# Kernel tuning notes

Measured on AMD Instinct MI355X. Metric: run time of the kernel, lower is better.

## Reference

```python
import jax, jax.numpy as jnp
import numpy as np
from jax import lax

KH, KW = 9, 9
FC_DIM = 1024
C_RED = FC_DIM // 8  # 128
EPS = 1e-5


def conv_bn_relu(x, w, gamma, beta):
    # 3x3 conv, stride 1, pad 1 (NCHW / OIHW), then batch-stat BN + ReLU
    y = lax.conv_general_dilated(x, w, (1, 1), ((1, 1), (1, 1)),
                                 dimension_numbers=('NCHW', 'OIHW', 'NCHW'))
    mean = y.mean(axis=(0, 2, 3))
    var = y.var(axis=(0, 2, 3))
    y = (y - mean[None, :, None, None]) * lax.rsqrt(var + EPS)[None, :, None, None]
    y = y * gamma[None, :, None, None] + beta[None, :, None, None]
    return jnp.maximum(y, 0.0)


def local_weighting(feat, atten, kH, kW):
    # feat: [B,C,H,W]; atten: [B,H,W,kH*kW]
    # out[b,c,h,w] = sum_k atten[b,h,w,k] * feat_padded[b,c,h+dh_k,w+dw_k]
    B, C, H, W = feat.shape
    ph, pw = kH // 2, kW // 2
    fp = jnp.pad(feat, ((0, 0), (0, 0), (ph, ph), (pw, pw)))
    out = jnp.zeros_like(feat)
    k = 0
    for dh in range(kH):
        for dw in range(kW):
            out = out + fp[:, :, dh:dh + H, dw:dw + W] * atten[:, None, :, :, k]
            k += 1
    return out


def setup_inputs() -> dict:
    key = jax.random.key(0)
    ks = jax.random.split(key, 12)
    B, H, W = 4, 64, 64
    sc1 = 1.0 / np.sqrt(FC_DIM * 9)
    sc5 = 1.0 / np.sqrt(C_RED * 9)
    return {
        'low_key': jax.random.normal(ks[0], (B, FC_DIM, H, W), jnp.float32),
        'low_nonkey': jax.random.normal(ks[1], (B, FC_DIM, H, W), jnp.float32),
        'local_atten': jax.random.uniform(ks[2], (B, H, W, KH * KW), jnp.float32),
        'w1': jax.random.normal(ks[3], (C_RED, FC_DIM, 3, 3), jnp.float32) * sc1,
        'g1': jnp.ones((C_RED,), jnp.float32),
        'b1': jnp.zeros((C_RED,), jnp.float32),
        'w4': jax.random.normal(ks[4], (C_RED, FC_DIM, 3, 3), jnp.float32) * sc1,
        'g4': jnp.ones((C_RED,), jnp.float32),
        'b4': jnp.zeros((C_RED,), jnp.float32),
        'w5': jax.random.normal(ks[5], (C_RED, C_RED, 3, 3), jnp.float32) * sc5,
        'g5': jnp.ones((C_RED,), jnp.float32),
        'b5': jnp.zeros((C_RED,), jnp.float32),
        'fc1_w': jax.random.normal(ks[6], (10, C_RED), jnp.float32) * (1.0 / np.sqrt(C_RED)),
        'fc1_b': jnp.zeros((10,), jnp.float32),
        'fc2_w': jax.random.normal(ks[7], (1, 10), jnp.float32) * (1.0 / np.sqrt(10.0)),
        'fc2_b': jnp.zeros((1,), jnp.float32),
    }


def reference(low_key, low_nonkey, local_atten,
              w1, g1, b1, w4, g4, b4, w5, g5, b5,
              fc1_w, fc1_b, fc2_w, fc2_b):
    lk = conv_bn_relu(low_key, w1, g1, b1)          # [B,128,H,W]
    trans = local_weighting(lk, local_atten, KH, KW)
    lnk = conv_bn_relu(low_nonkey, w4, g4, b4)
    out = trans - lnk
    out = conv_bn_relu(out, w5, g5, b5)
    out = out.mean(axis=(2, 3))                      # adaptive avg pool to 1x1 -> [B,128]
    out = out @ fc1_w.T + fc1_b
    out = out @ fc2_w.T + fc2_b                      # [B,1]
    return out
```

## Files before the change

kernel.cpp:

```cpp
#include <hip/hip_runtime.h>
#include <hip/hip_bf16.h>


#define B_ 4
#define CM_ 128

typedef __attribute__((ext_vector_type(8))) short short8;
typedef __attribute__((ext_vector_type(4))) float floatx4;
typedef __attribute__((address_space(3))) unsigned lds_as;
typedef __attribute__((address_space(1))) const unsigned glb_as;

__device__ inline short f2bf(float f) {
  union { float f; unsigned u; } v; v.f = f;
  unsigned r = v.u + 0x7fff + ((v.u >> 16) & 1);
  return (short)(r >> 16);
}
__device__ inline float bf2f(unsigned short u) {
  union { unsigned u; float f; } v; v.u = ((unsigned)u) << 16;
  return v.f;
}

template <int KB>
__global__ void xprep_kernel(const float* __restrict__ x, short* __restrict__ xt) {
  int kb = blockIdx.x >> 4, rg = blockIdx.x & 15;
  int b = blockIdx.y;
  int row = rg * 4 + (threadIdx.x >> 6);
  int col = threadIdx.x & 63;
  const float* xs = x + (((size_t)b * (KB * 32) + kb * 32) * 64 + row) * 64 + col;
  short* xd = xt + ((((size_t)b * KB + kb) * 64 + row) * 64 + col) * 32;
  int sw = (col >> 1) & 3;
#pragma unroll
  for (int u = 0; u < 4; u++) {
    short8 pk;
#pragma unroll
    for (int j = 0; j < 8; j++) pk[j] = f2bf(xs[(size_t)(u * 8 + j) * 4096]);
    *(short8*)(xd + (u ^ sw) * 8) = pk;
  }
}

__global__ void prep1_kernel(const float* __restrict__ x1,
                             const float* __restrict__ w1, const float* __restrict__ w4,
                             const float* __restrict__ w5, const float* __restrict__ atten,
                             short* __restrict__ xt, short* __restrict__ wf1,
                             short* __restrict__ wf4, short* __restrict__ wf5,
                             float* __restrict__ att_t, float* __restrict__ yz) {
  __shared__ float tile[5184];
  int bx = blockIdx.x, tid = threadIdx.x;
  if (bx < 2048) {
    int b = bx & 3, t = bx >> 2;
    int kb = t >> 4, rg = t & 15;
    int row = rg * 4 + (tid >> 6), col = tid & 63;
    const float* xs = x1 + (((size_t)b * 1024 + kb * 32) * 64 + row) * 64 + col;
    short* xd = xt + ((((size_t)b * 32 + kb) * 64 + row) * 64 + col) * 32;
    int sw = (col >> 1) & 3;
#pragma unroll
    for (int u = 0; u < 4; u++) {
      short8 pk;
#pragma unroll
      for (int j = 0; j < 8; j++) pk[j] = f2bf(xs[(size_t)(u * 8 + j) * 4096]);
      *(short8*)(xd + (u ^ sw) * 8) = pk;
    }
    return;
  }
  bx -= 2048;
  if (bx < 1024) {
    const float* w = bx < 512 ? w1 : w4;
    short* wf = bx < 512 ? wf1 : wf4;
    int idx = (bx & 511) * 256 + tid;
    int oc = idx >> 10, ic = idx & 1023;
    int kb = ic >> 5, icb = ic & 31, quad = icb >> 3, j = icb & 7;
    int m = oc >> 4, n16 = oc & 15, lane = quad * 16 + n16;
    const float* wp = w + ((size_t)oc * 1024 + ic) * 9;
    short* base = wf + (size_t)kb * 36864 + lane * 8 + j;
#pragma unroll
    for (int r = 0; r < 3; r++)
#pragma unroll
      for (int s = 0; s < 3; s++)
        base[(size_t)r * 12288 + (s * 8 + m) * 512] = f2bf(wp[r * 3 + s]);
    return;
  }
  bx -= 1024;
  if (bx < 64) {
    int idx = bx * 256 + tid;
    int oc = idx >> 7, ic = idx & 127;
    int kb = ic >> 5, icb = ic & 31, quad = icb >> 3, j = icb & 7;
    int m = oc >> 4, n16 = oc & 15, lane = quad * 16 + n16;
    const float* wp = w5 + ((size_t)oc * 128 + ic) * 9;
    short* base = wf5 + (size_t)kb * 36864 + lane * 8 + j;
#pragma unroll
    for (int r = 0; r < 3; r++)
#pragma unroll
      for (int s = 0; s < 3; s++)
        base[(size_t)r * 12288 + (s * 8 + m) * 512] = f2bf(wp[r * 3 + s]);
    return;
  }
  bx -= 64;
  if (bx < 256) {
    int b = bx >> 6;
    int p0 = (bx & 63) * 64;
    const float* src = atten + ((size_t)b * 4096 + p0) * 81;
    for (int e = tid; e < 5184; e += 256) tile[e] = src[e];
    __syncthreads();
    for (int f = tid; f < 5184; f += 256) {
      int k = f >> 6, w_ = f & 63;
      att_t[((size_t)b * 81 + k) * 4096 + p0 + w_] = tile[w_ * 81 + k];
    }
    return;
  }
  bx -= 256;
  ((float4*)yz)[(size_t)bx * 256 + tid] = make_float4(0.f, 0.f, 0.f, 0.f);
}

template <int KQ, bool ATOMIC>
__global__ __launch_bounds__(256, 2)
void convm_kernel(const short* __restrict__ xt, const short* __restrict__ wf,
                  float* __restrict__ ya, float* __restrict__ yb, int KBtot) {
  __shared__ __attribute__((aligned(16))) short smem[32768];
  int tid = threadIdx.x, lane = tid & 63, wv = tid >> 6;
  int n16 = lane & 15, quad = lane >> 4;
  int pg = blockIdx.x;
  int b = pg >> 5, h0 = (pg & 31) * 2;
  int kb0 = blockIdx.y * KQ;
  int mh = wv & 1, nh = wv >> 1;
  float* yo = ATOMIC ? ya : (blockIdx.y ? yb : ya);
  short* sx = smem + 24576;

  if (h0 == 0)
    for (int i = tid; i < 1024; i += 256) ((int*)sx)[i] = 0;
  if (h0 == 62)
    for (int i = tid; i < 1024; i += 256) ((int*)(sx + 3 * 2048))[i] = 0;

  auto dma_x = [&](int kb) {
    int row = h0 - 1 + wv;
    if (row >= 0 && row < 64) {
      const short* src = xt + ((((size_t)b * KBtot + kb) * 64 + row) * 64) * 32 + lane * 8;
      short* dst = sx + wv * 2048 + lane * 8;
#pragma unroll
      for (int t = 0; t < 4; t++)
        __builtin_amdgcn_global_load_lds((glb_as*)(src + t * 512), (lds_as*)(dst + t * 512),
                                         16, 0, 0);
    }
  };
  auto dma_w = [&](int step, int buf) {
    const short* src = wf + ((size_t)kb0 * 3 + step) * 12288 + wv * 3072 + lane * 8;
    short* dst = smem + buf * 12288 + wv * 3072 + lane * 8;
#pragma unroll
    for (int t = 0; t < 6; t++)
      __builtin_amdgcn_global_load_lds((glb_as*)(src + t * 512), (lds_as*)(dst + t * 512),
                                       16, 0, 0);
  };

  floatx4 acc[4][4];
#pragma unroll
  for (int i = 0; i < 4; i++)
#pragma unroll
    for (int n = 0; n < 4; n++) acc[i][n] = (floatx4){0.f, 0.f, 0.f, 0.f};

  dma_x(kb0);
  dma_w(0, 0);
  const int NS = KQ * 3;
  for (int s = 0; s < NS; s++) {
    int r = s % 3;
    __syncthreads();
    if (r == 0 && s > 0) {
      dma_x(kb0 + s / 3);
      if (s + 1 < NS) dma_w(s + 1, (s + 1) & 1);
      __syncthreads();
    } else {
      if (s + 1 < NS) dma_w(s + 1, (s + 1) & 1);
    }
    const short* swb = smem + (s & 1) * 12288;
    int slot = nh + r;
    const short* sxr = sx + slot * 2048;
#pragma unroll
    for (int sp = 0; sp < 3; sp++) {
      short8 a[4];
#pragma unroll
      for (int i = 0; i < 4; i++)
        a[i] = *(const short8*)(swb + ((sp * 8 + mh * 4 + i) * 64 + lane) * 8);
#pragma unroll
      for (int n = 0; n < 4; n++) {
        int c = n * 16 + n16 + sp - 1;
        int cc = c < 0 ? 0 : (c > 63 ? 63 : c);
        short8 bf = *(const short8*)(sxr + cc * 32 + (quad ^ ((cc >> 1) & 3)) * 8);
        if ((n == 0 && sp == 0) || (n == 3 && sp == 2)) {
          short8 zz = {0, 0, 0, 0, 0, 0, 0, 0};
          bf = (c != cc) ? zz : bf;
        }
#pragma unroll
        for (int i = 0; i < 4; i++)
          acc[i][n] = __builtin_amdgcn_mfma_f32_16x16x32_bf16(a[i], bf, acc[i][n], 0, 0, 0);
      }
    }
  }

  int row = h0 + nh;
#pragma unroll
  for (int i = 0; i < 4; i++)
#pragma unroll
    for (int n = 0; n < 4; n++)
#pragma unroll
      for (int rg = 0; rg < 4; rg++) {
        int oc = mh * 64 + i * 16 + quad * 4 + rg;
        size_t gi = (((size_t)b * CM_ + oc) * 64 + row) * 64 + n * 16 + n16;
        if (ATOMIC)
          atomicAdd(&yo[gi], acc[i][n][rg]);
        else
          yo[gi] = acc[i][n][rg];
      }
}

__global__ void bnstats2_kernel(const float* __restrict__ y1, const float* __restrict__ g1,
                                const float* __restrict__ b1, float2* __restrict__ s1,
                                const float* __restrict__ y4, const float* __restrict__ g4,
                                const float* __restrict__ b4, float2* __restrict__ s4) {
  const float* y = blockIdx.y ? y4 : y1;
  const float* g = blockIdx.y ? g4 : g1;
  const float* bt = blockIdx.y ? b4 : b1;
  float2* scsh = blockIdx.y ? s4 : s1;
  int c = blockIdx.x;
  int tid = threadIdx.x;
  float s = 0.f, s2 = 0.f;
  for (int b = 0; b < B_; b++) {
    const float4* p = (const float4*)(y + ((size_t)(b * CM_) + c) * 4096);
    for (int i = tid; i < 1024; i += 256) {
      float4 v = p[i];
      s += v.x + v.y + v.z + v.w;
      s2 += v.x * v.x + v.y * v.y + v.z * v.z + v.w * v.w;
    }
  }
  for (int off = 32; off > 0; off >>= 1) {
    s += __shfl_down(s, off);
    s2 += __shfl_down(s2, off);
  }
  __shared__ float rs[4], rq[4];
  if ((tid & 63) == 0) { rs[tid >> 6] = s; rq[tid >> 6] = s2; }
  __syncthreads();
  if (tid == 0) {
    float S = rs[0] + rs[1] + rs[2] + rs[3];
    float Q = rq[0] + rq[1] + rq[2] + rq[3];
    float mean = S * (1.f / 16384.f);
    float var = Q * (1.f / 16384.f) - mean * mean;
    float sc = g[c] * rsqrtf(var + 1e-5f);
    scsh[c] = make_float2(sc, bt[c] - mean * sc);
  }
}

__global__ void bnstats_s2_kernel(const float* __restrict__ ya, const float* __restrict__ yb,
                                  const float* __restrict__ g, const float* __restrict__ bt,
                                  float2* __restrict__ scsh) {
  int c = blockIdx.x;
  int tid = threadIdx.x;
  float s = 0.f, s2 = 0.f;
  for (int b = 0; b < B_; b++) {
    const float4* p = (const float4*)(ya + ((size_t)(b * CM_) + c) * 4096);
    const float4* q = (const float4*)(yb + ((size_t)(b * CM_) + c) * 4096);
    for (int i = tid; i < 1024; i += 256) {
      float4 v = p[i], w = q[i];
      float a0 = v.x + w.x, a1 = v.y + w.y, a2 = v.z + w.z, a3 = v.w + w.w;
      s += a0 + a1 + a2 + a3;
      s2 += a0 * a0 + a1 * a1 + a2 * a2 + a3 * a3;
    }
  }
  for (int off = 32; off > 0; off >>= 1) {
    s += __shfl_down(s, off);
    s2 += __shfl_down(s2, off);
  }
  __shared__ float rs[4], rq[4];
  if ((tid & 63) == 0) { rs[tid >> 6] = s; rq[tid >> 6] = s2; }
  __syncthreads();
  if (tid == 0) {
    float S = rs[0] + rs[1] + rs[2] + rs[3];
    float Q = rq[0] + rq[1] + rq[2] + rq[3];
    float mean = S * (1.f / 16384.f);
    float var = Q * (1.f / 16384.f) - mean * mean;
    float sc = g[c] * rsqrtf(var + 1e-5f);
    scsh[c] = make_float2(sc, bt[c] - mean * sc);
  }
}

__global__ __launch_bounds__(256, 2)
void localw_kernel(const float* __restrict__ y1, const float2* __restrict__ scsh1,
                   const float* __restrict__ y4, const float2* __restrict__ scsh4,
                   const float* __restrict__ att_t, short* __restrict__ xt5) {
  __shared__ unsigned short lkb[16][12][72];
  int bx = blockIdx.x;
  int b = bx >> 4, h0 = (bx & 15) * 4;
  int cg = blockIdx.y;
  int tid = threadIdx.x;
  int lane = tid & 63;
  int wv = tid >> 6;

  for (int e = tid; e < 16 * 12 * 72; e += 256) {
    int c_l = e / (12 * 72);
    int rem = e % (12 * 72);
    int gri = rem / 72, j = rem % 72;
    int row = h0 - 4 + gri, col = j - 4;
    float v = 0.f;
    if (row >= 0 && row < 64 && col >= 0 && col < 64) {
      float2 ss = scsh1[cg * 16 + c_l];
      v = fmaxf(0.f, y1[((size_t)(b * CM_) + cg * 16 + c_l) * 4096 + row * 64 + col] * ss.x + ss.y);
    }
    lkb[c_l][gri][j] = (unsigned short)f2bf(v);
  }
  __syncthreads();

  float acc[4][4];
#pragma unroll
  for (int cc = 0; cc < 4; cc++)
#pragma unroll
    for (int h_i = 0; h_i < 4; h_i++) acc[cc][h_i] = 0.f;

  const float* ab = att_t + (size_t)b * 81 * 4096 + h0 * 64 + lane;

#pragma unroll
  for (int gri = 0; gri < 12; ++gri) {
    float win[4][9];
#pragma unroll
    for (int cc = 0; cc < 4; ++cc)
#pragma unroll
      for (int dw = 0; dw < 9; ++dw)
        win[cc][dw] = bf2f(lkb[wv * 4 + cc][gri][lane + dw]);
#pragma unroll
    for (int h_i = 0; h_i < 4; ++h_i) {
      int r = gri - h_i;
      if (r < 0 || r > 8) continue;
      const float* ap = ab + (size_t)(r * 9) * 4096 + h_i * 64;
      float a[9];
#pragma unroll
      for (int dw = 0; dw < 9; ++dw) a[dw] = ap[(size_t)dw * 4096];
#pragma unroll
      for (int cc = 0; cc < 4; ++cc)
#pragma unroll
        for (int dw = 0; dw < 9; ++dw)
          acc[cc][h_i] = fmaf(a[dw], win[cc][dw], acc[cc][h_i]);
    }
  }

#pragma unroll
  for (int cc = 0; cc < 4; ++cc) {
    int c = cg * 16 + wv * 4 + cc;
    float2 ss4 = scsh4[c];
    int icb = c & 31;
    int uu = (icb >> 3) ^ ((lane >> 1) & 3);
#pragma unroll
    for (int h_i = 0; h_i < 4; ++h_i) {
      int h = h0 + h_i;
      size_t gi = ((size_t)(b * CM_) + c) * 4096 + h * 64 + lane;
      float lnk = fmaxf(0.f, y4[gi] * ss4.x + ss4.y);
      float dv = acc[cc][h_i] - lnk;
      xt5[((((size_t)b * 4 + (c >> 5)) * 64 + h) * 64 + lane) * 32 + uu * 8 + (icb & 7)] =
          f2bf(dv);
    }
  }
}

__global__ void pool_kernel(const float* __restrict__ ya, const float* __restrict__ yb,
                            const float2* __restrict__ scsh, float* __restrict__ pooled) {
  int bc = blockIdx.x;
  int c = bc & 127;
  float2 ss = scsh[c];
  const float4* p = (const float4*)(ya + (size_t)bc * 4096);
  const float4* q = (const float4*)(yb + (size_t)bc * 4096);
  float s = 0.f;
  for (int i = threadIdx.x; i < 1024; i += 256) {
    float4 v = p[i], w = q[i];
    s += fmaxf(0.f, (v.x + w.x) * ss.x + ss.y) + fmaxf(0.f, (v.y + w.y) * ss.x + ss.y) +
         fmaxf(0.f, (v.z + w.z) * ss.x + ss.y) + fmaxf(0.f, (v.w + w.w) * ss.x + ss.y);
  }
  for (int off = 32; off > 0; off >>= 1) s += __shfl_down(s, off);
  __shared__ float rs[4];
  if ((threadIdx.x & 63) == 0) rs[threadIdx.x >> 6] = s;
  __syncthreads();
  if (threadIdx.x == 0) pooled[bc] = (rs[0] + rs[1] + rs[2] + rs[3]) * (1.f / 4096.f);
}

__global__ void fc_kernel(const float* __restrict__ pooled, const float* __restrict__ fc1w,
                          const float* __restrict__ fc1b, const float* __restrict__ fc2w,
                          const float* __restrict__ fc2b, float* __restrict__ out) {
  int lane = threadIdx.x;
  float p[B_][10];
#pragma unroll
  for (int b = 0; b < B_; b++)
#pragma unroll
    for (int j = 0; j < 10; j++) p[b][j] = 0.f;
  for (int c = lane; c < CM_; c += 64) {
#pragma unroll
    for (int b = 0; b < B_; b++) {
      float pv = pooled[b * CM_ + c];
#pragma unroll
      for (int j = 0; j < 10; j++) p[b][j] = fmaf(pv, fc1w[j * CM_ + c], p[b][j]);
    }
  }
  for (int off = 32; off > 0; off >>= 1)
#pragma unroll
    for (int b = 0; b < B_; b++)
#pragma unroll
      for (int j = 0; j < 10; j++) p[b][j] += __shfl_down(p[b][j], off);
  if (lane == 0) {
    for (int b = 0; b < B_; b++) {
      float o = fc2b[0];
      for (int j = 0; j < 10; j++) o += fc2w[j] * (p[b][j] + fc1b[j]);
      out[b] = o;
    }
  }
}

extern "C" void kernel_launch(void* const* d_in, const int* in_sizes, int n_in,
                              void* d_out, int out_size, void* d_ws, size_t ws_size,
                              hipStream_t stream) {
  const float* low_key    = (const float*)d_in[0];
  const float* low_nonkey = (const float*)d_in[1];
  const float* atten      = (const float*)d_in[2];
  const float* w1  = (const float*)d_in[3];
  const float* g1  = (const float*)d_in[4];
  const float* b1  = (const float*)d_in[5];
  const float* w4  = (const float*)d_in[6];
  const float* g4  = (const float*)d_in[7];
  const float* b4  = (const float*)d_in[8];
  const float* w5  = (const float*)d_in[9];
  const float* g5  = (const float*)d_in[10];
  const float* b5  = (const float*)d_in[11];
  const float* fc1w = (const float*)d_in[12];
  const float* fc1b = (const float*)d_in[13];
  const float* fc2w = (const float*)d_in[14];
  const float* fc2b = (const float*)d_in[15];

  char* w8 = (char*)d_ws;
  short* wf1   = (short*)w8;
  short* wf4   = (short*)(w8 + 2359296);
  short* wf5   = (short*)(w8 + 4718592);
  float* att_t = (float*)(w8 + 5308416);
  short* xt    = (short*)(w8 + 10616832);
  float* y1    = (float*)(w8 + 44171264);
  float* y4    = (float*)(w8 + 52559872);
  float2* scsh1 = (float2*)(w8 + 60948480);
  float2* scsh4 = scsh1 + CM_;
  float2* scsh5 = scsh4 + CM_;
  float* pooled = (float*)(scsh5 + CM_);
  short* xt5 = xt;
  float* out = (float*)d_out;

  prep1_kernel<<<7488, 256, 0, stream>>>(low_key, w1, w4, w5, atten,
                                         xt, wf1, wf4, wf5, att_t, y1);
  convm_kernel<8, true><<<dim3(128, 4), 256, 0, stream>>>(xt, wf1, y1, y1, 32);
  xprep_kernel<32><<<dim3(512, 4), 256, 0, stream>>>(low_nonkey, xt);
  convm_kernel<8, true><<<dim3(128, 4), 256, 0, stream>>>(xt, wf4, y4, y4, 32);
  bnstats2_kernel<<<dim3(128, 2), 256, 0, stream>>>(y1, g1, b1, scsh1, y4, g4, b4, scsh4);
  localw_kernel<<<dim3(64, 8), 256, 0, stream>>>(y1, scsh1, y4, scsh4, att_t, xt5);
  convm_kernel<2, false><<<dim3(128, 2), 256, 0, stream>>>(xt5, wf5, y1, y4, 4);
  bnstats_s2_kernel<<<128, 256, 0, stream>>>(y1, y4, g5, b5, scsh5);
  pool_kernel<<<512, 256, 0, stream>>>(y1, y4, scsh5, pooled);
  fc_kernel<<<1, 64, 0, stream>>>(pooled, fc1w, fc1b, fc2w, fc2b, out);
}
```

Baseline: 387.4 us.

## Restructure conv pipeline into finer weight steps with double-buffered input tiles

The implicit-GEMM conv kernel now streams weights in nine small per-tap steps instead of three large ones, and double-buffers the input-row tiles so the next channel block loads while the current one computes. The smaller LDS footprint allows three blocks per CU, and the split-K factor doubles (more blocks, each over fewer channel blocks). The final conv switches to atomic accumulation into a buffer zeroed inside the localw kernel, so the later stats and pool kernels read one buffer instead of two. Trade-offs are more barriers per channel block, more atomic traffic, and register pressure under the tighter launch bound.

```diff
diff --git a/kernel.cpp b/kernel.cpp
--- a/kernel.cpp
+++ b/kernel.cpp
@@ -112,40 +112,44 @@
 }
 
 template <int KQ, bool ATOMIC>
-__global__ __launch_bounds__(256, 2)
+__global__ __launch_bounds__(256, 3)
 void convm_kernel(const short* __restrict__ xt, const short* __restrict__ wf,
-                  float* __restrict__ ya, float* __restrict__ yb, int KBtot) {
-  __shared__ __attribute__((aligned(16))) short smem[32768];
+                  float* __restrict__ yo, int KBtot) {
+  __shared__ __attribute__((aligned(16))) short smem[24576];
+  short* sw = smem;
+  short* sx = smem + 8192;
   int tid = threadIdx.x, lane = tid & 63, wv = tid >> 6;
   int n16 = lane & 15, quad = lane >> 4;
   int pg = blockIdx.x;
   int b = pg >> 5, h0 = (pg & 31) * 2;
   int kb0 = blockIdx.y * KQ;
   int mh = wv & 1, nh = wv >> 1;
-  float* yo = ATOMIC ? ya : (blockIdx.y ? yb : ya);
-  short* sx = smem + 24576;
 
   if (h0 == 0)
-    for (int i = tid; i < 1024; i += 256) ((int*)sx)[i] = 0;
+    for (int i = tid; i < 1024; i += 256) { ((int*)sx)[i] = 0; ((int*)(sx + 8192))[i] = 0; }
   if (h0 == 62)
-    for (int i = tid; i < 1024; i += 256) ((int*)(sx + 3 * 2048))[i] = 0;
-
-  auto dma_x = [&](int kb) {
+    for (int i = tid; i < 1024; i += 256) {
+      ((int*)(sx + 3 * 2048))[i] = 0;
+      ((int*)(sx + 8192 + 3 * 2048))[i] = 0;
+    }
+
+  auto dma_x = [&](int kbr) {
     int row = h0 - 1 + wv;
     if (row >= 0 && row < 64) {
-      const short* src = xt + ((((size_t)b * KBtot + kb) * 64 + row) * 64) * 32 + lane * 8;
-      short* dst = sx + wv * 2048 + lane * 8;
+      const short* src =
+          xt + ((((size_t)b * KBtot + kb0 + kbr) * 64 + row) * 64) * 32 + lane * 8;
+      short* dst = sx + (kbr & 1) * 8192 + wv * 2048 + lane * 8;
 #pragma unroll
       for (int t = 0; t < 4; t++)
         __builtin_amdgcn_global_load_lds((glb_as*)(src + t * 512), (lds_as*)(dst + t * 512),
                                          16, 0, 0);
     }
   };
-  auto dma_w = [&](int step, int buf) {
-    const short* src = wf + ((size_t)kb0 * 3 + step) * 12288 + wv * 3072 + lane * 8;
-    short* dst = smem + buf * 12288 + wv * 3072 + lane * 8;
-#pragma unroll
-    for (int t = 0; t < 6; t++)
+  auto dma_w = [&](int step) {
+    const short* src = wf + ((size_t)(kb0 * 9 + step)) * 4096 + wv * 1024 + lane * 8;
+    short* dst = sw + (step & 1) * 4096 + wv * 1024 + lane * 8;
+#pragma unroll
+    for (int t = 0; t < 2; t++)
       __builtin_amdgcn_global_load_lds((glb_as*)(src + t * 512), (lds_as*)(dst + t * 512),
                                        16, 0, 0);
   };
@@ -156,28 +160,23 @@
 #pragma unroll
     for (int n = 0; n < 4; n++) acc[i][n] = (floatx4){0.f, 0.f, 0.f, 0.f};
 
-  dma_x(kb0);
-  dma_w(0, 0);
-  const int NS = KQ * 3;
-  for (int s = 0; s < NS; s++) {
-    int r = s % 3;
-    __syncthreads();
-    if (r == 0 && s > 0) {
-      dma_x(kb0 + s / 3);
-      if (s + 1 < NS) dma_w(s + 1, (s + 1) & 1);
+  dma_x(0);
+  dma_w(0);
+  const int NS = KQ * 9;
+  for (int kb = 0; kb < KQ; kb++) {
+#pragma unroll
+    for (int rs = 0; rs < 9; rs++) {
+      int s = kb * 9 + rs;
       __syncthreads();
-    } else {
-      if (s + 1 < NS) dma_w(s + 1, (s + 1) & 1);
-    }
-    const short* swb = smem + (s & 1) * 12288;
-    int slot = nh + r;
-    const short* sxr = sx + slot * 2048;
-#pragma unroll
-    for (int sp = 0; sp < 3; sp++) {
+      if (s + 1 < NS) dma_w(s + 1);
+      if (rs == 0 && kb + 1 < KQ) dma_x(kb + 1);
+      int r = rs / 3, sp = rs % 3;
+      const short* swb = sw + (s & 1) * 4096;
+      const short* sxr = sx + (kb & 1) * 8192 + (nh + r) * 2048;
       short8 a[4];
 #pragma unroll
       for (int i = 0; i < 4; i++)
-        a[i] = *(const short8*)(swb + ((sp * 8 + mh * 4 + i) * 64 + lane) * 8);
+        a[i] = *(const short8*)(swb + ((mh * 4 + i) * 64 + lane) * 8);
 #pragma unroll
       for (int n = 0; n < 4; n++) {
         int c = n * 16 + n16 + sp - 1;
@@ -246,20 +245,17 @@
   }
 }
 
-__global__ void bnstats_s2_kernel(const float* __restrict__ ya, const float* __restrict__ yb,
-                                  const float* __restrict__ g, const float* __restrict__ bt,
-                                  float2* __restrict__ scsh) {
+__global__ void bnstats_kernel(const float* __restrict__ y, const float* __restrict__ g,
+                               const float* __restrict__ bt, float2* __restrict__ scsh) {
   int c = blockIdx.x;
   int tid = threadIdx.x;
   float s = 0.f, s2 = 0.f;
   for (int b = 0; b < B_; b++) {
-    const float4* p = (const float4*)(ya + ((size_t)(b * CM_) + c) * 4096);
-    const float4* q = (const float4*)(yb + ((size_t)(b * CM_) + c) * 4096);
+    const float4* p = (const float4*)(y + ((size_t)(b * CM_) + c) * 4096);
     for (int i = tid; i < 1024; i += 256) {
-      float4 v = p[i], w = q[i];
-      float a0 = v.x + w.x, a1 = v.y + w.y, a2 = v.z + w.z, a3 = v.w + w.w;
-      s += a0 + a1 + a2 + a3;
-      s2 += a0 * a0 + a1 * a1 + a2 * a2 + a3 * a3;
+      float4 v = p[i];
+      s += v.x + v.y + v.z + v.w;
+      s2 += v.x * v.x + v.y * v.y + v.z * v.z + v.w * v.w;
     }
   }
   for (int off = 32; off > 0; off >>= 1) {
@@ -282,7 +278,8 @@
 __global__ __launch_bounds__(256, 2)
 void localw_kernel(const float* __restrict__ y1, const float2* __restrict__ scsh1,
                    const float* __restrict__ y4, const float2* __restrict__ scsh4,
-                   const float* __restrict__ att_t, short* __restrict__ xt5) {
+                   const float* __restrict__ att_t, short* __restrict__ xt5,
+                   float* __restrict__ y5z) {
   __shared__ unsigned short lkb[16][12][72];
   int bx = blockIdx.x;
   int b = bx >> 4, h0 = (bx & 15) * 4;
@@ -290,6 +287,14 @@
   int tid = threadIdx.x;
   int lane = tid & 63;
   int wv = tid >> 6;
+
+  {
+    float4* z = (float4*)y5z;
+    int bid = cg * 64 + bx;
+#pragma unroll
+    for (int t = 0; t < 4; t++)
+      z[(size_t)bid * 1024 + t * 256 + tid] = make_float4(0.f, 0.f, 0.f, 0.f);
+  }
 
   for (int e = tid; e < 16 * 12 * 72; e += 256) {
     int c_l = e / (12 * 72);
@@ -355,18 +360,17 @@
   }
 }
 
-__global__ void pool_kernel(const float* __restrict__ ya, const float* __restrict__ yb,
-                            const float2* __restrict__ scsh, float* __restrict__ pooled) {
+__global__ void pool_kernel(const float* __restrict__ y, const float2* __restrict__ scsh,
+                            float* __restrict__ pooled) {
   int bc = blockIdx.x;
   int c = bc & 127;
   float2 ss = scsh[c];
-  const float4* p = (const float4*)(ya + (size_t)bc * 4096);
-  const float4* q = (const float4*)(yb + (size_t)bc * 4096);
+  const float4* p = (const float4*)(y + (size_t)bc * 4096);
   float s = 0.f;
   for (int i = threadIdx.x; i < 1024; i += 256) {
-    float4 v = p[i], w = q[i];
-    s += fmaxf(0.f, (v.x + w.x) * ss.x + ss.y) + fmaxf(0.f, (v.y + w.y) * ss.x + ss.y) +
-         fmaxf(0.f, (v.z + w.z) * ss.x + ss.y) + fmaxf(0.f, (v.w + w.w) * ss.x + ss.y);
+    float4 v = p[i];
+    s += fmaxf(0.f, v.x * ss.x + ss.y) + fmaxf(0.f, v.y * ss.x + ss.y) +
+         fmaxf(0.f, v.z * ss.x + ss.y) + fmaxf(0.f, v.w * ss.x + ss.y);
   }
   for (int off = 32; off > 0; off >>= 1) s += __shfl_down(s, off);
   __shared__ float rs[4];
@@ -439,17 +443,18 @@
   float2* scsh5 = scsh4 + CM_;
   float* pooled = (float*)(scsh5 + CM_);
   short* xt5 = xt;
+  float* y5  = (float*)(w8 + 10616832 + 8388608);
   float* out = (float*)d_out;
 
   prep1_kernel<<<7488, 256, 0, stream>>>(low_key, w1, w4, w5, atten,
                                          xt, wf1, wf4, wf5, att_t, y1);
-  convm_kernel<8, true><<<dim3(128, 4), 256, 0, stream>>>(xt, wf1, y1, y1, 32);
+  convm_kernel<4, true><<<dim3(128, 8), 256, 0, stream>>>(xt, wf1, y1, 32);
   xprep_kernel<32><<<dim3(512, 4), 256, 0, stream>>>(low_nonkey, xt);
-  convm_kernel<8, true><<<dim3(128, 4), 256, 0, stream>>>(xt, wf4, y4, y4, 32);
+  convm_kernel<4, true><<<dim3(128, 8), 256, 0, stream>>>(xt, wf4, y4, 32);
   bnstats2_kernel<<<dim3(128, 2), 256, 0, stream>>>(y1, g1, b1, scsh1, y4, g4, b4, scsh4);
-  localw_kernel<<<dim3(64, 8), 256, 0, stream>>>(y1, scsh1, y4, scsh4, att_t, xt5);
-  convm_kernel<2, false><<<dim3(128, 2), 256, 0, stream>>>(xt5, wf5, y1, y4, 4);
-  bnstats_s2_kernel<<<128, 256, 0, stream>>>(y1, y4, g5, b5, scsh5);
-  pool_kernel<<<512, 256, 0, stream>>>(y1, y4, scsh5, pooled);
+  localw_kernel<<<dim3(64, 8), 256, 0, stream>>>(y1, scsh1, y4, scsh4, att_t, xt5, y5);
+  convm_kernel<1, true><<<dim3(128, 4), 256, 0, stream>>>(xt5, wf5, y5, 4);
+  bnstats_kernel<<<128, 256, 0, stream>>>(y5, g5, b5, scsh5);
+  pool_kernel<<<512, 256, 0, stream>>>(y5, scsh5, pooled);
   fc_kernel<<<1, 64, 0, stream>>>(pooled, fc1w, fc1b, fc2w, fc2b, out);
 }
```

Measured after the change: 441.3 us. 1.14x slower.
